# Kernel tuning notes

Hardware: AMD Instinct MI355X
Metric: run time of the kernel (lower is better)

The kernel has to match this reference:

```python
import jax, jax.numpy as jnp
import numpy as np

DIM = 4096
NUM_EXPERTS = 64
TOP_K = 8
TOKENS = 16384

def setup_inputs() -> dict:
    key = jax.random.key(0)
    kx, kw = jax.random.split(key)
    x = jax.random.normal(kx, (TOKENS, DIM), dtype=jnp.float32)
    # gate weight as in nn.Linear(dim, num_experts, bias=False): shape [num_experts, dim]
    W = jax.random.normal(kw, (NUM_EXPERTS, DIM), dtype=jnp.float32) * 0.02
    return {"x": x, "W": W}

def reference(x, W):
    # logits = x @ W^T : [tokens, num_experts]
    logits = jnp.einsum('td,ed->te', x, W)
    top_k_values, top_k_indices = jax.lax.top_k(logits, TOP_K)
    # softmax over top-k values in float32, cast back to x dtype
    scores = jax.nn.softmax(top_k_values.astype(jnp.float32), axis=-1).astype(x.dtype)
    return scores, top_k_indices
```

## Files before the change

kernel.cpp:

```cpp
#include <hip/hip_runtime.h>
#include <math.h>

typedef float  f32x4 __attribute__((ext_vector_type(4)));
typedef short  s16x8 __attribute__((ext_vector_type(8)));
typedef unsigned short u16x8 __attribute__((ext_vector_type(8)));

constexpr int TOKENS  = 16384;
constexpr int DIM     = 4096;
constexpr int NE      = 64;
constexpr int TOPK    = 8;
constexpr int TM      = 64;
constexpr int KB      = 32;
constexpr int NIT     = DIM / KB;
constexpr int LISTCAP = 16384;
constexpr float GAPTH = 1e-4f;

__device__ __forceinline__ unsigned short bf_rne(float f) {
    unsigned u = __float_as_uint(f);
    u += 0x7FFFu + ((u >> 16) & 1u);
    return (unsigned short)(u >> 16);
}
__device__ __forceinline__ float bf_f32(unsigned short h) {
    return __uint_as_float(((unsigned)h) << 16);
}

__global__ void zero_cnt_kernel(int* wsI) { if (threadIdx.x == 0) wsI[0] = 0; }

__global__ __launch_bounds__(256)
void gemm_topk_kernel(const float* __restrict__ x, const float* __restrict__ W,
                      float* __restrict__ out, int* __restrict__ wsI)
{
    __shared__ __align__(16) unsigned short frag[8192];
    __shared__ float ls[TM][NE + 4];

    const int t    = threadIdx.x;
    const int tok0 = blockIdx.x * TM;

    const int srow = t >> 2;
    const int sq   = t & 3;
    const int sn   = srow & 15;
    const int sT   = srow >> 4;
    const int sdst = sT * 512 + (16 * sq + (sn ^ (2 * sq))) * 8;
    const float* xg = x + (size_t)(tok0 + srow) * DIM + 8 * sq;
    const float* wg = W + (size_t)srow * DIM + 8 * sq;

    const int w  = t >> 6;
    const int l  = t & 63;
    const int lq = l >> 4;
    const int ln = l & 15;
    const int fo = (16 * lq + (ln ^ (2 * lq))) * 8;

    f32x4 acc[4];
#pragma unroll
    for (int T = 0; T < 4; ++T) acc[T] = (f32x4){0.f, 0.f, 0.f, 0.f};

    float4 xa = *(const float4*)xg;
    float4 xb = *(const float4*)(xg + 4);
    float4 wa = *(const float4*)wg;
    float4 wb = *(const float4*)(wg + 4);

    for (int it = 0; it < NIT; ++it) {
        __syncthreads();
        {
            float vx[8] = {xa.x, xa.y, xa.z, xa.w, xb.x, xb.y, xb.z, xb.w};
            float vw[8] = {wa.x, wa.y, wa.z, wa.w, wb.x, wb.y, wb.z, wb.w};
            u16x8 vxh, vxl, vwh, vwl;
#pragma unroll
            for (int j = 0; j < 8; ++j) {
                unsigned short h1 = bf_rne(vx[j]);
                vxh[j] = h1;
                vxl[j] = bf_rne(vx[j] - bf_f32(h1));
                unsigned short h2 = bf_rne(vw[j]);
                vwh[j] = h2;
                vwl[j] = bf_rne(vw[j] - bf_f32(h2));
            }
            *(u16x8*)&frag[   0 + sdst] = vxh;
            *(u16x8*)&frag[2048 + sdst] = vxl;
            *(u16x8*)&frag[4096 + sdst] = vwh;
            *(u16x8*)&frag[6144 + sdst] = vwl;
        }
        __syncthreads();
        if (it + 1 < NIT) {
            const float* xp = xg + (size_t)(it + 1) * KB;
            const float* wp = wg + (size_t)(it + 1) * KB;
            xa = *(const float4*)xp;  xb = *(const float4*)(xp + 4);
            wa = *(const float4*)wp;  wb = *(const float4*)(wp + 4);
        }
        s16x8 ah = *(const s16x8*)&frag[   0 + w * 512 + fo];
        s16x8 al = *(const s16x8*)&frag[2048 + w * 512 + fo];
#pragma unroll
        for (int T = 0; T < 4; ++T) {
            s16x8 bh = *(const s16x8*)&frag[4096 + T * 512 + fo];
            s16x8 bl = *(const s16x8*)&frag[6144 + T * 512 + fo];
            acc[T] = __builtin_amdgcn_mfma_f32_16x16x32_bf16(ah, bh, acc[T], 0, 0, 0);
            acc[T] = __builtin_amdgcn_mfma_f32_16x16x32_bf16(ah, bl, acc[T], 0, 0, 0);
            acc[T] = __builtin_amdgcn_mfma_f32_16x16x32_bf16(al, bh, acc[T], 0, 0, 0);
        }
    }

    __syncthreads();
#pragma unroll
    for (int T = 0; T < 4; ++T)
#pragma unroll
        for (int r = 0; r < 4; ++r)
            ls[16 * w + 4 * lq + r][16 * T + ln] = acc[T][r];
    __syncthreads();

    if (t < TM) {
        const int tok = tok0 + t;
        float v[9]; int idx[9];
#pragma unroll
        for (int j = 0; j < 9; ++j) {
            float best = -3.4e38f; int bi = 0;
            for (int e = 0; e < NE; ++e) {
                float q = ls[t][e];
                if (q > best) { best = q; bi = e; }
            }
            v[j] = best; idx[j] = bi;
            ls[t][bi] = -3.4e38f;
        }
        bool flag = false;
#pragma unroll
        for (int j = 0; j < 8; ++j)
            if (v[j] - v[j + 1] < GAPTH) flag = true;

        float m = v[0], s = 0.f, ex[8];
#pragma unroll
        for (int j = 0; j < 8; ++j) { ex[j] = expf(v[j] - m); s += ex[j]; }
        float inv = 1.f / s;
#pragma unroll
        for (int j = 0; j < 8; ++j) {
            out[(size_t)tok * TOPK + j] = ex[j] * inv;
            out[(size_t)TOKENS * TOPK + (size_t)tok * TOPK + j] = (float)idx[j];
        }
        if (flag) {
            int pos = atomicAdd(wsI, 1);
            if (pos < LISTCAP) wsI[16 + pos] = tok;
        }
    }
}

__global__ __launch_bounds__(256)
void refine_kernel(const float* __restrict__ x, const float* __restrict__ W,
                   float* __restrict__ out, const int* __restrict__ wsI)
{
    __shared__ float  xr[DIM];
    __shared__ double pt[256];
    __shared__ double lg[NE];

    int cnt = wsI[0];
    if (cnt > LISTCAP) cnt = LISTCAP;
    const int t = threadIdx.x;

    for (int g = blockIdx.x; g < cnt; g += gridDim.x) {
        const int tok = wsI[16 + g];
        __syncthreads();
        for (int i = t; i < DIM / 4; i += 256)
            *(float4*)&xr[4 * i] = *(const float4*)&x[(size_t)tok * DIM + 4 * i];
        __syncthreads();

        const int e  = t & 63;
        const int ks = t >> 6;
        const float* wp = W + (size_t)e * DIM + ks * 1024;
        const float* xp = xr + ks * 1024;
        double p = 0.0;
        for (int i = 0; i < 256; ++i) {
            float4 wv = *(const float4*)&wp[4 * i];
            float4 xv = *(const float4*)&xp[4 * i];
            p = fma((double)xv.x, (double)wv.x, p);
            p = fma((double)xv.y, (double)wv.y, p);
            p = fma((double)xv.z, (double)wv.z, p);
            p = fma((double)xv.w, (double)wv.w, p);
        }
        pt[t] = p;
        __syncthreads();
        if (t < NE)
            lg[t] = ((pt[t] + pt[t + 64]) + pt[t + 128]) + pt[t + 192];
        __syncthreads();
        if (t == 0) {
            double vv[8]; int ii[8];
#pragma unroll
            for (int j = 0; j < 8; ++j) {
                double best = -1e300; int bi = 0;
                for (int e2 = 0; e2 < NE; ++e2) {
                    double q = lg[e2];
                    if (q > best) { best = q; bi = e2; }
                }
                vv[j] = best; ii[j] = bi;
                lg[bi] = -1e300;
            }
            float pf[8], ex[8], s = 0.f;
#pragma unroll
            for (int j = 0; j < 8; ++j) pf[j] = (float)vv[j];
            float m = pf[0];
#pragma unroll
            for (int j = 0; j < 8; ++j) { ex[j] = expf(pf[j] - m); s += ex[j]; }
            float inv = 1.f / s;
#pragma unroll
            for (int j = 0; j < 8; ++j) {
                out[(size_t)tok * TOPK + j] = ex[j] * inv;
                out[(size_t)TOKENS * TOPK + (size_t)tok * TOPK + j] = (float)ii[j];
            }
        }
    }
}

extern "C" void kernel_launch(void* const* d_in, const int* in_sizes, int n_in,
                              void* d_out, int out_size, void* d_ws, size_t ws_size,
                              hipStream_t stream)
{
    const float* x = (const float*)d_in[0];
    const float* W = (const float*)d_in[1];
    float* out = (float*)d_out;
    int* wsI = (int*)d_ws;

    hipLaunchKernelGGL(zero_cnt_kernel, dim3(1), dim3(64), 0, stream, wsI);
    hipLaunchKernelGGL(gemm_topk_kernel, dim3(TOKENS / TM), dim3(256), 0, stream, x, W, out, wsI);
    hipLaunchKernelGGL(refine_kernel, dim3(256), dim3(256), 0, stream, x, W, out, wsI);
}
```

Baseline: 485.7 us.

## Pre-split W into bf16 fragment layout and load MFMA operands directly from global

Adds a pre-pass kernel that converts W into hi/lo bf16 pairs stored in MFMA fragment order in workspace, so the main GEMM no longer converts W each iteration. The new GEMM drops shared-memory staging and barriers, loads x straight into registers, converts it in registers, and software-prefetches the next iterations. It also shrinks blocks to 32 tokens and 128 threads with two blocks per CU. This removes the LDS round trips and synchronisation from the hot loop, at the cost of more global loads of W per block and extra workspace. The old path is kept as a fallback for when the workspace is too small.

```diff
diff --git a/kernel.cpp b/kernel.cpp
--- a/kernel.cpp
+++ b/kernel.cpp
@@ -4,17 +4,21 @@
 typedef float  f32x4 __attribute__((ext_vector_type(4)));
 typedef short  s16x8 __attribute__((ext_vector_type(8)));
 typedef unsigned short u16x8 __attribute__((ext_vector_type(8)));
+typedef unsigned int   u32x4 __attribute__((ext_vector_type(4)));
 
 constexpr int TOKENS  = 16384;
 constexpr int DIM     = 4096;
 constexpr int NE      = 64;
 constexpr int TOPK    = 8;
-constexpr int TM      = 64;
 constexpr int KB      = 32;
 constexpr int NIT     = DIM / KB;
 constexpr int LISTCAP = 16384;
 constexpr float GAPTH = 1e-4f;
 
+constexpr unsigned WARR_U16   = (unsigned)NIT * 4 * 64 * 8;
+constexpr size_t   WS_INT_OFF = (size_t)WARR_U16 * 2 * sizeof(unsigned short);
+constexpr size_t   WS_NEEDED  = WS_INT_OFF + sizeof(int) * (size_t)(16 + LISTCAP);
+
 __device__ __forceinline__ unsigned short bf_rne(float f) {
     unsigned u = __float_as_uint(f);
     u += 0x7FFFu + ((u >> 16) & 1u);
@@ -23,82 +27,103 @@
 __device__ __forceinline__ float bf_f32(unsigned short h) {
     return __uint_as_float(((unsigned)h) << 16);
 }
-
-__global__ void zero_cnt_kernel(int* wsI) { if (threadIdx.x == 0) wsI[0] = 0; }
+__device__ __forceinline__ uint2 cvt_pair(float f0, float f1) {
+    unsigned short h0 = bf_rne(f0);
+    unsigned short h1 = bf_rne(f1);
+    uint2 r;
+    r.x = (unsigned)h0 | ((unsigned)h1 << 16);
+    r.y = (unsigned)bf_rne(f0 - bf_f32(h0)) | ((unsigned)bf_rne(f1 - bf_f32(h1)) << 16);
+    return r;
+}
+union Cvt { u32x4 u; s16x8 s; };
 
 __global__ __launch_bounds__(256)
-void gemm_topk_kernel(const float* __restrict__ x, const float* __restrict__ W,
-                      float* __restrict__ out, int* __restrict__ wsI)
-{
-    __shared__ __align__(16) unsigned short frag[8192];
-    __shared__ float ls[TM][NE + 4];
+void wconv_kernel(const float* __restrict__ W, unsigned short* __restrict__ wpk,
+                  int* __restrict__ wsI)
+{
+    unsigned tid = blockIdx.x * 256u + threadIdx.x;
+    if (tid == 0) wsI[0] = 0;
+    unsigned j    = tid & 7u;
+    unsigned lane = (tid >> 3) & 63u;
+    unsigned T    = (tid >> 9) & 3u;
+    unsigned it   = tid >> 11;
+    unsigned e = 16u * T + (lane & 15u);
+    unsigned k = 32u * it + 8u * (lane >> 4) + j;
+    float v = W[(size_t)e * DIM + k];
+    unsigned short h = bf_rne(v);
+    wpk[tid]            = h;
+    wpk[WARR_U16 + tid] = bf_rne(v - bf_f32(h));
+}
+
+__global__ __launch_bounds__(128, 2)
+void gemm_topk_v2(const float* __restrict__ x,
+                  const unsigned short* __restrict__ wpk,
+                  float* __restrict__ out, int* __restrict__ wsI)
+{
+    __shared__ float ls[32][NE + 4];
 
     const int t    = threadIdx.x;
-    const int tok0 = blockIdx.x * TM;
-
-    const int srow = t >> 2;
-    const int sq   = t & 3;
-    const int sn   = srow & 15;
-    const int sT   = srow >> 4;
-    const int sdst = sT * 512 + (16 * sq + (sn ^ (2 * sq))) * 8;
-    const float* xg = x + (size_t)(tok0 + srow) * DIM + 8 * sq;
-    const float* wg = W + (size_t)srow * DIM + 8 * sq;
-
-    const int w  = t >> 6;
-    const int l  = t & 63;
-    const int lq = l >> 4;
-    const int ln = l & 15;
-    const int fo = (16 * lq + (ln ^ (2 * lq))) * 8;
+    const int w    = t >> 6;
+    const int l    = t & 63;
+    const int lq   = l >> 4;
+    const int ln   = l & 15;
+    const int tok0 = blockIdx.x * 32;
+
+    const float* xg = x + (size_t)(tok0 + 16 * w + ln) * DIM + 8 * lq;
+    const s16x8* bhp = (const s16x8*)wpk + l;
+    const s16x8* blp = bhp + (WARR_U16 / 8);
 
     f32x4 acc[4];
 #pragma unroll
     for (int T = 0; T < 4; ++T) acc[T] = (f32x4){0.f, 0.f, 0.f, 0.f};
 
-    float4 xa = *(const float4*)xg;
-    float4 xb = *(const float4*)(xg + 4);
-    float4 wa = *(const float4*)wg;
-    float4 wb = *(const float4*)(wg + 4);
-
+    float4 xa0 = *(const float4*)(xg + 0);
+    float4 xa1 = *(const float4*)(xg + 4);
+    float4 xb0 = *(const float4*)(xg + KB + 0);
+    float4 xb1 = *(const float4*)(xg + KB + 4);
+    s16x8 bh0 = bhp[0], bh1 = bhp[64], bh2 = bhp[128], bh3 = bhp[192];
+    s16x8 bl0 = blp[0], bl1 = blp[64], bl2 = blp[128], bl3 = blp[192];
+
+#pragma unroll 2
     for (int it = 0; it < NIT; ++it) {
-        __syncthreads();
-        {
-            float vx[8] = {xa.x, xa.y, xa.z, xa.w, xb.x, xb.y, xb.z, xb.w};
-            float vw[8] = {wa.x, wa.y, wa.z, wa.w, wb.x, wb.y, wb.z, wb.w};
-            u16x8 vxh, vxl, vwh, vwl;
-#pragma unroll
-            for (int j = 0; j < 8; ++j) {
-                unsigned short h1 = bf_rne(vx[j]);
-                vxh[j] = h1;
-                vxl[j] = bf_rne(vx[j] - bf_f32(h1));
-                unsigned short h2 = bf_rne(vw[j]);
-                vwh[j] = h2;
-                vwl[j] = bf_rne(vw[j] - bf_f32(h2));
-            }
-            *(u16x8*)&frag[   0 + sdst] = vxh;
-            *(u16x8*)&frag[2048 + sdst] = vxl;
-            *(u16x8*)&frag[4096 + sdst] = vwh;
-            *(u16x8*)&frag[6144 + sdst] = vwl;
-        }
-        __syncthreads();
-        if (it + 1 < NIT) {
-            const float* xp = xg + (size_t)(it + 1) * KB;
-            const float* wp = wg + (size_t)(it + 1) * KB;
-            xa = *(const float4*)xp;  xb = *(const float4*)(xp + 4);
-            wa = *(const float4*)wp;  wb = *(const float4*)(wp + 4);
-        }
-        s16x8 ah = *(const s16x8*)&frag[   0 + w * 512 + fo];
-        s16x8 al = *(const s16x8*)&frag[2048 + w * 512 + fo];
-#pragma unroll
-        for (int T = 0; T < 4; ++T) {
-            s16x8 bh = *(const s16x8*)&frag[4096 + T * 512 + fo];
-            s16x8 bl = *(const s16x8*)&frag[6144 + T * 512 + fo];
-            acc[T] = __builtin_amdgcn_mfma_f32_16x16x32_bf16(ah, bh, acc[T], 0, 0, 0);
-            acc[T] = __builtin_amdgcn_mfma_f32_16x16x32_bf16(ah, bl, acc[T], 0, 0, 0);
-            acc[T] = __builtin_amdgcn_mfma_f32_16x16x32_bf16(al, bh, acc[T], 0, 0, 0);
-        }
-    }
-
-    __syncthreads();
+        const int itx = (it + 2 < NIT) ? it + 2 : NIT - 1;
+        const float* xp = xg + (size_t)KB * itx;
+        float4 xn0 = *(const float4*)(xp + 0);
+        float4 xn1 = *(const float4*)(xp + 4);
+
+        const int itn = (it + 1 < NIT) ? it + 1 : NIT - 1;
+        const s16x8* nhp = bhp + itn * 256;
+        const s16x8* nlp = blp + itn * 256;
+        s16x8 nh0 = nhp[0], nh1 = nhp[64], nh2 = nhp[128], nh3 = nhp[192];
+        s16x8 nl0 = nlp[0], nl1 = nlp[64], nl2 = nlp[128], nl3 = nlp[192];
+
+        uint2 p0 = cvt_pair(xa0.x, xa0.y);
+        uint2 p1 = cvt_pair(xa0.z, xa0.w);
+        uint2 p2 = cvt_pair(xa1.x, xa1.y);
+        uint2 p3 = cvt_pair(xa1.z, xa1.w);
+        Cvt ch, cl;
+        ch.u = (u32x4){p0.x, p1.x, p2.x, p3.x};
+        cl.u = (u32x4){p0.y, p1.y, p2.y, p3.y};
+        s16x8 ah = ch.s, al = cl.s;
+
+        acc[0] = __builtin_amdgcn_mfma_f32_16x16x32_bf16(ah, bh0, acc[0], 0, 0, 0);
+        acc[1] = __builtin_amdgcn_mfma_f32_16x16x32_bf16(ah, bh1, acc[1], 0, 0, 0);
+        acc[2] = __builtin_amdgcn_mfma_f32_16x16x32_bf16(ah, bh2, acc[2], 0, 0, 0);
+        acc[3] = __builtin_amdgcn_mfma_f32_16x16x32_bf16(ah, bh3, acc[3], 0, 0, 0);
+        acc[0] = __builtin_amdgcn_mfma_f32_16x16x32_bf16(ah, bl0, acc[0], 0, 0, 0);
+        acc[1] = __builtin_amdgcn_mfma_f32_16x16x32_bf16(ah, bl1, acc[1], 0, 0, 0);
+        acc[2] = __builtin_amdgcn_mfma_f32_16x16x32_bf16(ah, bl2, acc[2], 0, 0, 0);
+        acc[3] = __builtin_amdgcn_mfma_f32_16x16x32_bf16(ah, bl3, acc[3], 0, 0, 0);
+        acc[0] = __builtin_amdgcn_mfma_f32_16x16x32_bf16(al, bh0, acc[0], 0, 0, 0);
+        acc[1] = __builtin_amdgcn_mfma_f32_16x16x32_bf16(al, bh1, acc[1], 0, 0, 0);
+        acc[2] = __builtin_amdgcn_mfma_f32_16x16x32_bf16(al, bh2, acc[2], 0, 0, 0);
+        acc[3] = __builtin_amdgcn_mfma_f32_16x16x32_bf16(al, bh3, acc[3], 0, 0, 0);
+
+        bh0 = nh0; bh1 = nh1; bh2 = nh2; bh3 = nh3;
+        bl0 = nl0; bl1 = nl1; bl2 = nl2; bl3 = nl3;
+        xa0 = xb0; xa1 = xb1; xb0 = xn0; xb1 = xn1;
+    }
+
 #pragma unroll
     for (int T = 0; T < 4; ++T)
 #pragma unroll
@@ -106,18 +131,19 @@
             ls[16 * w + 4 * lq + r][16 * T + ln] = acc[T][r];
     __syncthreads();
 
-    if (t < TM) {
-        const int tok = tok0 + t;
+    if ((t & 3) == 0) {
+        const int ti  = t >> 2;
+        const int tok = tok0 + ti;
         float v[9]; int idx[9];
 #pragma unroll
         for (int j = 0; j < 9; ++j) {
             float best = -3.4e38f; int bi = 0;
             for (int e = 0; e < NE; ++e) {
-                float q = ls[t][e];
+                float q = ls[ti][e];
                 if (q > best) { best = q; bi = e; }
             }
             v[j] = best; idx[j] = bi;
-            ls[t][bi] = -3.4e38f;
+            ls[ti][bi] = -3.4e38f;
         }
         bool flag = false;
 #pragma unroll
@@ -205,6 +231,122 @@
     }
 }
 
+__global__ void zero_cnt_kernel(int* wsI) { if (threadIdx.x == 0) wsI[0] = 0; }
+
+__global__ __launch_bounds__(256)
+void gemm_topk_old(const float* __restrict__ x, const float* __restrict__ W,
+                   float* __restrict__ out, int* __restrict__ wsI)
+{
+    __shared__ __align__(16) unsigned short frag[8192];
+    __shared__ float ls[64][NE + 4];
+
+    const int t    = threadIdx.x;
+    const int tok0 = blockIdx.x * 64;
+
+    const int srow = t >> 2;
+    const int sq   = t & 3;
+    const int sn   = srow & 15;
+    const int sT   = srow >> 4;
+    const int sdst = sT * 512 + (16 * sq + (sn ^ (2 * sq))) * 8;
+    const float* xg = x + (size_t)(tok0 + srow) * DIM + 8 * sq;
+    const float* wg = W + (size_t)srow * DIM + 8 * sq;
+
+    const int w  = t >> 6;
+    const int l  = t & 63;
+    const int lq = l >> 4;
+    const int ln = l & 15;
+    const int fo = (16 * lq + (ln ^ (2 * lq))) * 8;
+
+    f32x4 acc[4];
+#pragma unroll
+    for (int T = 0; T < 4; ++T) acc[T] = (f32x4){0.f, 0.f, 0.f, 0.f};
+
+    float4 xa = *(const float4*)xg;
+    float4 xb = *(const float4*)(xg + 4);
+    float4 wa = *(const float4*)wg;
+    float4 wb = *(const float4*)(wg + 4);
+
+    for (int it = 0; it < NIT; ++it) {
+        __syncthreads();
+        {
+            float vx[8] = {xa.x, xa.y, xa.z, xa.w, xb.x, xb.y, xb.z, xb.w};
+            float vw[8] = {wa.x, wa.y, wa.z, wa.w, wb.x, wb.y, wb.z, wb.w};
+            u16x8 vxh, vxl, vwh, vwl;
+#pragma unroll
+            for (int j = 0; j < 8; ++j) {
+                unsigned short h1 = bf_rne(vx[j]);
+                vxh[j] = h1;
+                vxl[j] = bf_rne(vx[j] - bf_f32(h1));
+                unsigned short h2 = bf_rne(vw[j]);
+                vwh[j] = h2;
+                vwl[j] = bf_rne(vw[j] - bf_f32(h2));
+            }
+            *(u16x8*)&frag[   0 + sdst] = vxh;
+            *(u16x8*)&frag[2048 + sdst] = vxl;
+            *(u16x8*)&frag[4096 + sdst] = vwh;
+            *(u16x8*)&frag[6144 + sdst] = vwl;
+        }
+        __syncthreads();
+        if (it + 1 < NIT) {
+            const float* xp = xg + (size_t)(it + 1) * KB;
+            const float* wp = wg + (size_t)(it + 1) * KB;
+            xa = *(const float4*)xp;  xb = *(const float4*)(xp + 4);
+            wa = *(const float4*)wp;  wb = *(const float4*)(wp + 4);
+        }
+        s16x8 ah = *(const s16x8*)&frag[   0 + w * 512 + fo];
+        s16x8 al = *(const s16x8*)&frag[2048 + w * 512 + fo];
+#pragma unroll
+        for (int T = 0; T < 4; ++T) {
+            s16x8 bh = *(const s16x8*)&frag[4096 + T * 512 + fo];
+            s16x8 bl = *(const s16x8*)&frag[6144 + T * 512 + fo];
+            acc[T] = __builtin_amdgcn_mfma_f32_16x16x32_bf16(ah, bh, acc[T], 0, 0, 0);
+            acc[T] = __builtin_amdgcn_mfma_f32_16x16x32_bf16(ah, bl, acc[T], 0, 0, 0);
+            acc[T] = __builtin_amdgcn_mfma_f32_16x16x32_bf16(al, bh, acc[T], 0, 0, 0);
+        }
+    }
+
+    __syncthreads();
+#pragma unroll
+    for (int T = 0; T < 4; ++T)
+#pragma unroll
+        for (int r = 0; r < 4; ++r)
+            ls[16 * w + 4 * lq + r][16 * T + ln] = acc[T][r];
+    __syncthreads();
+
+    if (t < 64) {
+        const int tok = tok0 + t;
+        float v[9]; int idx[9];
+#pragma unroll
+        for (int j = 0; j < 9; ++j) {
+            float best = -3.4e38f; int bi = 0;
+            for (int e = 0; e < NE; ++e) {
+                float q = ls[t][e];
+                if (q > best) { best = q; bi = e; }
+            }
+            v[j] = best; idx[j] = bi;
+            ls[t][bi] = -3.4e38f;
+        }
+        bool flag = false;
+#pragma unroll
+        for (int j = 0; j < 8; ++j)
+            if (v[j] - v[j + 1] < GAPTH) flag = true;
+
+        float m = v[0], s = 0.f, ex[8];
+#pragma unroll
+        for (int j = 0; j < 8; ++j) { ex[j] = expf(v[j] - m); s += ex[j]; }
+        float inv = 1.f / s;
+#pragma unroll
+        for (int j = 0; j < 8; ++j) {
+            out[(size_t)tok * TOPK + j] = ex[j] * inv;
+            out[(size_t)TOKENS * TOPK + (size_t)tok * TOPK + j] = (float)idx[j];
+        }
+        if (flag) {
+            int pos = atomicAdd(wsI, 1);
+            if (pos < LISTCAP) wsI[16 + pos] = tok;
+        }
+    }
+}
+
 extern "C" void kernel_launch(void* const* d_in, const int* in_sizes, int n_in,
                               void* d_out, int out_size, void* d_ws, size_t ws_size,
                               hipStream_t stream)
@@ -212,9 +354,17 @@
     const float* x = (const float*)d_in[0];
     const float* W = (const float*)d_in[1];
     float* out = (float*)d_out;
-    int* wsI = (int*)d_ws;
-
-    hipLaunchKernelGGL(zero_cnt_kernel, dim3(1), dim3(64), 0, stream, wsI);
-    hipLaunchKernelGGL(gemm_topk_kernel, dim3(TOKENS / TM), dim3(256), 0, stream, x, W, out, wsI);
-    hipLaunchKernelGGL(refine_kernel, dim3(256), dim3(256), 0, stream, x, W, out, wsI);
-}
+
+    if (ws_size >= WS_NEEDED) {
+        unsigned short* wpk = (unsigned short*)d_ws;
+        int* wsI = (int*)((char*)d_ws + WS_INT_OFF);
+        hipLaunchKernelGGL(wconv_kernel, dim3(WARR_U16 / 256), dim3(256), 0, stream, W, wpk, wsI);
+        hipLaunchKernelGGL(gemm_topk_v2, dim3(TOKENS / 32), dim3(128), 0, stream, x, wpk, out, wsI);
+        hipLaunchKernelGGL(refine_kernel, dim3(256), dim3(256), 0, stream, x, W, out, wsI);
+    } else {
+        int* wsI = (int*)d_ws;
+        hipLaunchKernelGGL(zero_cnt_kernel, dim3(1), dim3(64), 0, stream, wsI);
+        hipLaunchKernelGGL(gemm_topk_old, dim3(TOKENS / 64), dim3(256), 0, stream, x, W, out, wsI);
+        hipLaunchKernelGGL(refine_kernel, dim3(256), dim3(256), 0, stream, x, W, out, wsI);
+    }
+}
```

Result: slower. 503.9 us (+3.7%).
